# Kernel optimization log

Measured on AMD Instinct MI355X. Metric: run time of the kernel, lower is better.

## Reference

```python
import jax, jax.numpy as jnp
import numpy as np

RES = 128
STEPSIZE = 0.5
NEAR, FAR, BG = 0.2, 3.0, 1.0
ALPHA_INIT = 0.01
XYZ_MIN, XYZ_MAX = -1.0, 1.0
N_RAYS = 1024
RGB_LATENT = 15
MULTIRES = 6
EMB_DIM = 3 + 3 * 2 * MULTIRES  # 39
DIM0 = RGB_LATENT + EMB_DIM     # 54
VOXEL = (XYZ_MAX - XYZ_MIN) / RES  # ((2^3)/RES^3)^(1/3)
N_SAMPLES = int(np.linalg.norm(np.array([RES] * 3) * 2 + 1) / STEPSIZE) + 1  # 891
ACT_SHIFT = float(np.log(1.0 / (1.0 - ALPHA_INIT) - 1.0))


def embed_dirs(d):
    # NeRF positional encoding, include_inputs=True, multires=6 -> 39 dims
    freqs = 2.0 ** jnp.arange(MULTIRES, dtype=d.dtype)
    ang = d[..., None, :] * freqs[:, None]  # [M,6,3]
    return jnp.concatenate([d, jnp.sin(ang).reshape(d.shape[0], -1), jnp.cos(ang).reshape(d.shape[0], -1)], -1)


def grid_sample3d(g, coords):
    # g: [C,D,H,W]; coords: [M,3] in (-1,1), torch grid_sample convention
    # (comp0 -> W axis, comp1 -> H axis, comp2 -> D axis), align_corners=True,
    # border-clamped indices (sampled out-of-box points are masked out anyway).
    C, D, H, W = g.shape
    x = (coords[:, 0] + 1) * 0.5 * (W - 1)
    y = (coords[:, 1] + 1) * 0.5 * (H - 1)
    z = (coords[:, 2] + 1) * 0.5 * (D - 1)
    x0, y0, z0 = jnp.floor(x), jnp.floor(y), jnp.floor(z)
    fx, fy, fz = x - x0, y - y0, z - z0
    x0i = jnp.clip(x0.astype(jnp.int32), 0, W - 1); x1i = jnp.clip(x0i + 1, 0, W - 1)
    y0i = jnp.clip(y0.astype(jnp.int32), 0, H - 1); y1i = jnp.clip(y0i + 1, 0, H - 1)
    z0i = jnp.clip(z0.astype(jnp.int32), 0, D - 1); z1i = jnp.clip(z0i + 1, 0, D - 1)
    gf = g.reshape(C, -1)
    def gv(zi, yi, xi):
        return gf[:, (zi * H + yi) * W + xi]  # [C,M]
    c = (((gv(z0i, y0i, x0i) * (1 - fx) + gv(z0i, y0i, x1i) * fx) * (1 - fy)
          + (gv(z0i, y1i, x0i) * (1 - fx) + gv(z0i, y1i, x1i) * fx) * fy) * (1 - fz)
         + ((gv(z1i, y0i, x0i) * (1 - fx) + gv(z1i, y0i, x1i) * fx) * (1 - fy)
            + (gv(z1i, y1i, x0i) * (1 - fx) + gv(z1i, y1i, x1i) * fx) * fy) * fz)
    return c.T  # [M,C]


def _forward(rays_o, rays_d, viewdirs, grid, sobel_kernel, w0, b0, w1, b1, w2, b2, w3, b3):
    # --- sample_ray: ray/AABB intersection + uniform stepping ---
    vec = jnp.where(rays_d == 0, 1e-6, rays_d)
    rate_a = (XYZ_MAX - rays_o) / vec
    rate_b = (XYZ_MIN - rays_o) / vec
    t_min = jnp.clip(jnp.minimum(rate_a, rate_b).max(-1), NEAR, FAR)
    t_max = jnp.clip(jnp.maximum(rate_a, rate_b).min(-1), NEAR, FAR)
    mask_ray = t_max <= t_min
    rng = jnp.arange(N_SAMPLES, dtype=rays_o.dtype)[None]
    step = STEPSIZE * VOXEL * rng
    interpx = t_min[:, None] + step / jnp.linalg.norm(rays_d, axis=-1, keepdims=True)
    pts = rays_o[:, None, :] + rays_d[:, None, :] * interpx[..., None]  # [N,S,3]
    inbox = (~mask_ray[:, None]) & (~((pts < XYZ_MIN) | (pts > XYZ_MAX)).any(-1))
    mflat = inbox.reshape(-1)

    # --- sobel normals grid (GridReg.forward(calc_normals=True)) ---
    density_grid = grid[None, :1]  # [1,1,D,H,W]
    nrm = jax.lax.conv_general_dilated(density_grid, sobel_kernel, (1, 1, 1), [(2, 2)] * 3,
                                       dimension_numbers=('NCDHW', 'OIDHW', 'NCDHW'))  # [1,3,D,H,W]
    nrm = -nrm / jnp.maximum(jnp.linalg.norm(nrm, axis=1, keepdims=True), 1e-12)
    normals_grid = nrm[0]

    # --- extract_latent: trilinear sample at ray points (masked via where) ---
    flat = pts.reshape(-1, 3)
    coords = ((flat - XYZ_MIN) / (XYZ_MAX - XYZ_MIN))[:, ::-1] * 2 - 1  # flip xyz->zyx
    lat = grid_sample3d(grid, coords)          # [M,16]
    ns = grid_sample3d(normals_grid, coords)   # [M,3]
    ns = -ns / jnp.maximum(jnp.linalg.norm(ns, axis=-1, keepdims=True), 1e-12)

    alpha = jnp.where(mflat, 1 - jnp.exp(-jax.nn.softplus(lat[:, 0] + ACT_SHIFT) * STEPSIZE), 0.0)
    alpha = alpha.reshape(N_RAYS, N_SAMPLES)
    normals = jnp.where(mflat[:, None], ns, 0.0).reshape(N_RAYS, N_SAMPLES, 3)
    rgb_lat = jnp.where(mflat[:, None], lat[:, 1:], 0.0)  # [M,15]

    # --- alpha compositing (cumprod_exclusive / get_ray_marching_ray) ---
    alphainv_cum = jnp.concatenate([jnp.ones_like(alpha[:, :1]),
                                    jnp.cumprod(jnp.maximum(1 - alpha, 1e-10), -1)], -1)
    weights = alpha * alphainv_cum[:, :-1]

    # --- reflected-direction shading MLP ---
    v = jnp.broadcast_to(viewdirs[:, None, :], normals.shape)
    dot = jnp.sum(-v * normals, -1, keepdims=True)
    refdirs = (2 * dot * normals + v).reshape(-1, 3)
    feat = jnp.concatenate([rgb_lat, embed_dirs(refdirs)], -1)  # [M,54]
    h = jax.nn.relu(feat @ w0 + b0)
    h = jax.nn.relu(h @ w1 + b1)
    h = jax.nn.relu(h @ w2 + b2)
    col = jax.nn.sigmoid(h @ w3 + b3)
    rgb = jnp.where(mflat[:, None], col, 0.0).reshape(N_RAYS, N_SAMPLES, 3)

    rgb_marched = (weights[..., None] * rgb).sum(-2) + alphainv_cum[:, -1:] * BG
    return rgb_marched


def setup_inputs() -> dict:
    key = jax.random.key(0)
    ks = jax.random.split(key, 8)
    rays_o = 0.3 * jax.random.normal(ks[0], (N_RAYS, 3), jnp.float32)
    rd = jax.random.normal(ks[1], (N_RAYS, 3), jnp.float32)
    rays_d = rd / jnp.linalg.norm(rd, axis=-1, keepdims=True)
    grid = 0.1 * jax.random.normal(ks[2], (1 + RGB_LATENT, RES, RES, RES), jnp.float32)
    sobel_kernel = jax.random.normal(ks[3], (3, 1, 5, 5, 5), jnp.float32)
    def lin(k, i, o):
        return jax.random.normal(k, (i, o), jnp.float32) / np.sqrt(i).astype(np.float32)
    return {
        'rays_o': rays_o, 'rays_d': rays_d, 'viewdirs': rays_d,
        'grid': grid, 'sobel_kernel': sobel_kernel,
        'w0': lin(ks[4], DIM0, 64), 'b0': jnp.zeros((64,), jnp.float32),
        'w1': lin(ks[5], 64, 64), 'b1': jnp.zeros((64,), jnp.float32),
        'w2': lin(ks[6], 64, 64), 'b2': jnp.zeros((64,), jnp.float32),
        'w3': lin(ks[7], 64, 3), 'b3': jnp.zeros((3,), jnp.float32),
    }


def reference(rays_o, rays_d, viewdirs, grid, sobel_kernel, w0, b0, w1, b1, w2, b2, w3, b3):
    return _forward(rays_o, rays_d, viewdirs, grid, sobel_kernel, w0, b0, w1, b1, w2, b2, w3, b3)
```

## Files before the change

### kernel.cpp

```cpp
#include <hip/hip_runtime.h>
#include <hip/hip_bf16.h>
#include <hip/hip_fp16.h>
#include <math.h>

#define RESV 128
#define V3 (RESV*RESV*RESV)
#define N_RAYS 1024
#define N_SAMPLES 891
#define STEP_T 0.0078125f
#define ACT_SHIFT -4.595119850134589f

typedef short bf16x8 __attribute__((ext_vector_type(8)));
typedef float f32x4 __attribute__((ext_vector_type(4)));

__device__ __forceinline__ unsigned short f2b(float x) {
    unsigned int u = __float_as_uint(x);
    unsigned int r = (u + 0x7FFFu + ((u >> 16) & 1u)) >> 16;
    return (unsigned short)r;
}

__device__ __forceinline__ void acc2(float w, unsigned int u, float& lo, float& hi) {
    lo = fmaf(w, __uint_as_float(u << 16), lo);
    hi = fmaf(w, __uint_as_float(u & 0xffff0000u), hi);
}

#define ROWS 60
#define ZSTR 136

__global__ __launch_bounds__(256)
void normals_conv_kernel(const float* __restrict__ grid,
                         const float* __restrict__ sobel,
                         float4* __restrict__ nrm4) {
    __shared__ float sk[375];
    __shared__ __align__(16) float tile[ROWS * ZSTR];

    const int t = threadIdx.x;
    const int bx = blockIdx.x;
    const int ix = bx >> 4;
    const int iy0 = (bx & 15) * 8;

    for (int i = t; i < 375; i += 256) sk[i] = sobel[i];

    {
        const int lane32 = t & 31;
        for (int r = t >> 5; r < ROWS; r += 8) {
            const int xl = r / 12, yl = r % 12;
            const int gx = ix + xl - 2;
            const int gy = iy0 + yl - 2;
            float4 v = make_float4(0.f, 0.f, 0.f, 0.f);
            if ((unsigned)gx < 128u && (unsigned)gy < 128u)
                v = *(const float4*)&grid[(size_t)(gx * 128 + gy) * 128 + lane32 * 4];
            *(float4*)&tile[r * ZSTR + 4 + lane32 * 4] = v;
        }
        if (t < ROWS) {
            float* row = tile + t * ZSTR;
            row[0] = 0.f; row[1] = 0.f; row[2] = 0.f; row[3] = 0.f;
            row[132] = 0.f; row[133] = 0.f; row[134] = 0.f; row[135] = 0.f;
        }
    }
    __syncthreads();

    const int iz4 = (t & 31) * 4;
    const int iyl = t >> 5;

    float c0[4] = {0.f, 0.f, 0.f, 0.f};
    float c1[4] = {0.f, 0.f, 0.f, 0.f};
    float c2[4] = {0.f, 0.f, 0.f, 0.f};

    #pragma unroll
    for (int da = 0; da < 5; ++da) {
        #pragma unroll
        for (int db = 0; db < 5; ++db) {
            const float* row = tile + (da * 12 + iyl + db + 2) * ZSTR;
            const float* k0  = sk + (da * 5 + db) * 5;
            float gbuf[12];
            *(float4*)&gbuf[0] = *(const float4*)&row[iz4];
            *(float4*)&gbuf[4] = *(const float4*)&row[iz4 + 4];
            *(float4*)&gbuf[8] = *(const float4*)&row[iz4 + 8];
            #pragma unroll
            for (int zz = 0; zz < 4; ++zz) {
                #pragma unroll
                for (int dc = 0; dc < 5; ++dc) {
                    const float gv = gbuf[2 + zz + dc];
                    c0[zz] = fmaf(gv, k0[dc],       c0[zz]);
                    c1[zz] = fmaf(gv, k0[125 + dc], c1[zz]);
                    c2[zz] = fmaf(gv, k0[250 + dc], c2[zz]);
                }
            }
        }
    }
    const int vbase = (ix * 128 + iy0 + iyl) * 128 + iz4;
    #pragma unroll
    for (int zz = 0; zz < 4; ++zz) {
        float l   = sqrtf(c0[zz]*c0[zz] + c1[zz]*c1[zz] + c2[zz]*c2[zz]);
        float inv = -1.0f / fmaxf(l, 1e-12f);
        nrm4[vbase + zz] = make_float4(c0[zz]*inv, c1[zz]*inv, c2[zz]*inv, 0.f);
    }
}

__global__ __launch_bounds__(256)
void repack_kernel(const float* __restrict__ grid,
                   unsigned short* __restrict__ latp) {
    const int i = blockIdx.x * 256 + threadIdx.x;
    const int v0 = i * 4;
    unsigned int r[4][8];
    #pragma unroll
    for (int c = 0; c < 16; c += 2) {
        const float4 a = *(const float4*)&grid[(size_t)c * V3 + v0];
        const float4 b = *(const float4*)&grid[(size_t)(c + 1) * V3 + v0];
        const float* pa = &a.x; const float* pb = &b.x;
        #pragma unroll
        for (int z = 0; z < 4; ++z)
            r[z][c >> 1] = (unsigned int)f2b(pa[z]) | ((unsigned int)f2b(pb[z]) << 16);
    }
    uint4* d = (uint4*)&latp[(size_t)v0 * 16];
    #pragma unroll
    for (int z = 0; z < 4; ++z) {
        d[z * 2 + 0] = make_uint4(r[z][0], r[z][1], r[z][2], r[z][3]);
        d[z * 2 + 1] = make_uint4(r[z][4], r[z][5], r[z][6], r[z][7]);
    }
}

__device__ __forceinline__ void mfma_layer(unsigned short* __restrict__ actw,
                                           const unsigned short* __restrict__ WT,
                                           const float* __restrict__ Bv,
                                           int r16, int q4, int q8) {
    f32x4 acc[4][4];
    #pragma unroll
    for (int nb = 0; nb < 4; ++nb) {
        const float bv = Bv[nb * 16 + r16];
        #pragma unroll
        for (int mb = 0; mb < 4; ++mb) {
            acc[mb][nb][0] = bv; acc[mb][nb][1] = bv;
            acc[mb][nb][2] = bv; acc[mb][nb][3] = bv;
        }
    }
    #pragma unroll
    for (int ks = 0; ks < 2; ++ks) {
        bf16x8 Af[4], Bf[4];
        #pragma unroll
        for (int mb = 0; mb < 4; ++mb)
            Af[mb] = *(const bf16x8*)&actw[(mb * 16 + r16) * 72 + ks * 32 + q8];
        #pragma unroll
        for (int nb = 0; nb < 4; ++nb)
            Bf[nb] = *(const bf16x8*)&WT[(nb * 16 + r16) * 72 + ks * 32 + q8];
        #pragma unroll
        for (int mb = 0; mb < 4; ++mb) {
            #pragma unroll
            for (int nb = 0; nb < 4; ++nb)
                acc[mb][nb] = __builtin_amdgcn_mfma_f32_16x16x32_bf16(
                    Af[mb], Bf[nb], acc[mb][nb], 0, 0, 0);
        }
    }
    #pragma unroll
    for (int mb = 0; mb < 4; ++mb) {
        #pragma unroll
        for (int nb = 0; nb < 4; ++nb) {
            #pragma unroll
            for (int r = 0; r < 4; ++r) {
                const int row = mb * 16 + q4 + r;
                actw[row * 72 + nb * 16 + r16] = f2b(fmaxf(acc[mb][nb][r], 0.f));
            }
        }
    }
}

#define WT0_OFF 0
#define WT1_OFF (64*72)
#define WT2_OFF (128*72)
#define WT3_OFF (192*72)

template <bool PL>
__global__ __launch_bounds__(256)
void raymarch_kernel(const float* __restrict__ ro, const float* __restrict__ rd,
                     const float* __restrict__ vd, const float* __restrict__ grid,
                     const float4* __restrict__ nrm4,
                     const unsigned short* __restrict__ latp,
                     const float* __restrict__ w0, const float* __restrict__ b0,
                     const float* __restrict__ w1, const float* __restrict__ b1,
                     const float* __restrict__ w2, const float* __restrict__ b2,
                     const float* __restrict__ w3, const float* __restrict__ b3,
                     float* __restrict__ out) {
    __shared__ __align__(16) unsigned short sWT[208 * 72];
    __shared__ __align__(16) unsigned short act[4 * 64 * 72];
    __shared__ float sb0f[64], sb1f[64], sb2f[64], sb3f[16];
    __shared__ __half salpha[1024];
    __shared__ __half scr[1024], scg[1024], scb[1024];
    __shared__ float lgl[1024];
    __shared__ float aux[256];
    __shared__ float red[12];

    const int t = threadIdx.x;
    const int ray = blockIdx.x;
    const int lane = t & 63;
    const int wave = t >> 6;
    const int r16 = lane & 15;
    const int q4 = (lane >> 4) * 4;
    const int q8 = (lane >> 4) * 8;
    unsigned short* const actw = act + wave * 64 * 72;

    for (int i = t; i < 64 * 72; i += 256) {
        int o = i / 72, k = i % 72;
        sWT[WT0_OFF + i] = f2b((k < 54) ? w0[k * 64 + o] : 0.f);
        sWT[WT1_OFF + i] = f2b((k < 64) ? w1[k * 64 + o] : 0.f);
        sWT[WT2_OFF + i] = f2b((k < 64) ? w2[k * 64 + o] : 0.f);
    }
    for (int i = t; i < 16 * 72; i += 256) {
        int n = i / 72, k = i % 72;
        sWT[WT3_OFF + i] = f2b((n < 3 && k < 64) ? w3[k * 3 + n] : 0.f);
    }
    if (t < 64) { sb0f[t] = b0[t]; sb1f[t] = b1[t]; sb2f[t] = b2[t]; }
    if (t < 16) sb3f[t] = (t < 3) ? b3[t] : 0.f;
    __syncthreads();

    const float ox = ro[ray * 3 + 0], oy = ro[ray * 3 + 1], oz = ro[ray * 3 + 2];
    const float dx = rd[ray * 3 + 0], dyv = rd[ray * 3 + 1], dzv = rd[ray * 3 + 2];
    const float vx = vd[ray * 3 + 0], vy = vd[ray * 3 + 1], vz = vd[ray * 3 + 2];

    const float ex = (dx  == 0.f) ? 1e-6f : dx;
    const float ey = (dyv == 0.f) ? 1e-6f : dyv;
    const float ez = (dzv == 0.f) ? 1e-6f : dzv;
    const float rax = (1.f - ox) / ex, rbx = (-1.f - ox) / ex;
    const float ray_ = (1.f - oy) / ey, rby = (-1.f - oy) / ey;
    const float raz = (1.f - oz) / ez, rbz = (-1.f - oz) / ez;
    float tmin = fmaxf(fmaxf(fminf(rax, rbx), fminf(ray_, rby)), fminf(raz, rbz));
    float tmax = fminf(fminf(fmaxf(rax, rbx), fmaxf(ray_, rby)), fmaxf(raz, rbz));
    tmin = fminf(fmaxf(tmin, 0.2f), 3.0f);
    tmax = fminf(fmaxf(tmax, 0.2f), 3.0f);
    const bool mask_ray = (tmax <= tmin);
    const float invn = 1.0f / sqrtf(dx * dx + dyv * dyv + dzv * dzv);

    #pragma unroll 1
    for (int j = 0; j < 4; ++j) {
        const int s = j * 256 + t;
        float alpha_s = 0.f;
        bool active = (s < N_SAMPLES) && !mask_ray;
        float px = 0.f, py = 0.f, pz = 0.f;
        if (active) {
            const float ti = tmin + STEP_T * (float)s * invn;
            px = fmaf(dx, ti, ox);
            py = fmaf(dyv, ti, oy);
            pz = fmaf(dzv, ti, oz);
            active = !(px < -1.f || px > 1.f || py < -1.f || py > 1.f ||
                       pz < -1.f || pz > 1.f);
        }
        const unsigned long long wmask = __ballot(active);
        if (wmask == 0ull) {
            salpha[s] = __float2half(0.f);
            lgl[s] = 0.f;
            scr[s] = __float2half(0.f); scg[s] = __float2half(0.f);
            scb[s] = __float2half(0.f);
            continue;
        }

        float feat[54];
        #pragma unroll
        for (int i = 0; i < 54; ++i) feat[i] = 0.f;

        if (active) {
            const float ga = (px + 1.f) * 63.5f;
            const float gb = (py + 1.f) * 63.5f;
            const float gc = (pz + 1.f) * 63.5f;
            const float fla = floorf(ga), flb = floorf(gb), flc = floorf(gc);
            const float fa = ga - fla, fb = gb - flb, fc = gc - flc;
            int ia0 = min(max((int)fla, 0), 127);
            int ib0 = min(max((int)flb, 0), 127);
            int ic0 = min(max((int)flc, 0), 127);
            int ia1 = min(ia0 + 1, 127);
            int ib1 = min(ib0 + 1, 127);
            int ic1 = min(ic0 + 1, 127);
            const int base00 = (ia0 * 128 + ib0) * 128;
            const int base01 = (ia0 * 128 + ib1) * 128;
            const int base10 = (ia1 * 128 + ib0) * 128;
            const int base11 = (ia1 * 128 + ib1) * 128;
            int idxs[8] = { base00 + ic0, base00 + ic1, base01 + ic0, base01 + ic1,
                            base10 + ic0, base10 + ic1, base11 + ic0, base11 + ic1 };
            const float wa0 = 1.f - fa, wb0 = 1.f - fb, wc0 = 1.f - fc;
            float w8[8] = { wa0*wb0*wc0, wa0*wb0*fc, wa0*fb*wc0, wa0*fb*fc,
                            fa*wb0*wc0,  fa*wb0*fc,  fa*fb*wc0,  fa*fb*fc };

            float lat[16];
            #pragma unroll
            for (int c = 0; c < 16; ++c) lat[c] = 0.f;
            if constexpr (PL) {
                #pragma unroll
                for (int k = 0; k < 8; ++k) {
                    const uint4* rec = (const uint4*)&latp[(size_t)idxs[k] * 16];
                    const uint4 u0 = rec[0];
                    const uint4 u1 = rec[1];
                    const float w = w8[k];
                    acc2(w, u0.x, lat[0],  lat[1]);
                    acc2(w, u0.y, lat[2],  lat[3]);
                    acc2(w, u0.z, lat[4],  lat[5]);
                    acc2(w, u0.w, lat[6],  lat[7]);
                    acc2(w, u1.x, lat[8],  lat[9]);
                    acc2(w, u1.y, lat[10], lat[11]);
                    acc2(w, u1.z, lat[12], lat[13]);
                    acc2(w, u1.w, lat[14], lat[15]);
                }
            } else {
                #pragma unroll
                for (int c = 0; c < 16; ++c) {
                    const float* gcp = grid + (size_t)c * V3;
                    float acc = 0.f;
                    #pragma unroll
                    for (int k = 0; k < 8; ++k) acc = fmaf(w8[k], gcp[idxs[k]], acc);
                    lat[c] = acc;
                }
            }
            const float lat0 = lat[0];
            #pragma unroll
            for (int c = 0; c < 15; ++c) feat[c] = lat[c + 1];

            float n0 = 0.f, n1 = 0.f, n2 = 0.f;
            #pragma unroll
            for (int k = 0; k < 8; ++k) {
                const float4 nv = nrm4[idxs[k]];
                n0 = fmaf(w8[k], nv.x, n0);
                n1 = fmaf(w8[k], nv.y, n1);
                n2 = fmaf(w8[k], nv.z, n2);
            }
            const float nl = sqrtf(n0*n0 + n1*n1 + n2*n2);
            const float ninv = -1.0f / fmaxf(nl, 1e-12f);
            n0 *= ninv; n1 *= ninv; n2 *= ninv;
            const float dotv = -(vx * n0 + vy * n1 + vz * n2);
            const float rx = fmaf(2.f * dotv, n0, vx);
            const float ry = fmaf(2.f * dotv, n1, vy);
            const float rz = fmaf(2.f * dotv, n2, vz);

            const float d0 = lat0 + ACT_SHIFT;
            const float sp = (d0 > 20.f) ? d0 : __logf(1.f + __expf(d0));
            alpha_s = 1.f - __expf(-sp * 0.5f);

            feat[15] = rx; feat[16] = ry; feat[17] = rz;
            float fr = 1.f;
            #pragma unroll
            for (int k = 0; k < 6; ++k) {
                feat[18 + k*3 + 0] = __sinf(rx * fr);
                feat[18 + k*3 + 1] = __sinf(ry * fr);
                feat[18 + k*3 + 2] = __sinf(rz * fr);
                feat[36 + k*3 + 0] = __cosf(rx * fr);
                feat[36 + k*3 + 1] = __cosf(ry * fr);
                feat[36 + k*3 + 2] = __cosf(rz * fr);
                fr *= 2.f;
            }
        }
        salpha[s] = __float2half(alpha_s);
        lgl[s] = __logf(fmaxf(1.f - alpha_s, 1e-10f));

        unsigned int* arow = (unsigned int*)&act[(size_t)t * 72];
        #pragma unroll
        for (int p = 0; p < 27; ++p)
            arow[p] = (unsigned int)f2b(feat[2*p]) |
                      ((unsigned int)f2b(feat[2*p + 1]) << 16);
        #pragma unroll
        for (int p = 27; p < 32; ++p) arow[p] = 0u;

        mfma_layer(actw, sWT + WT0_OFF, sb0f, r16, q4, q8);
        mfma_layer(actw, sWT + WT1_OFF, sb1f, r16, q4, q8);
        mfma_layer(actw, sWT + WT2_OFF, sb2f, r16, q4, q8);

        {
            f32x4 acch[4];
            const float bv = sb3f[r16];
            #pragma unroll
            for (int mb = 0; mb < 4; ++mb) {
                acch[mb][0] = bv; acch[mb][1] = bv;
                acch[mb][2] = bv; acch[mb][3] = bv;
            }
            #pragma unroll
            for (int ks = 0; ks < 2; ++ks) {
                const bf16x8 Bh = *(const bf16x8*)&sWT[WT3_OFF + r16 * 72 + ks * 32 + q8];
                #pragma unroll
                for (int mb = 0; mb < 4; ++mb) {
                    const bf16x8 Af = *(const bf16x8*)&actw[(mb * 16 + r16) * 72 + ks * 32 + q8];
                    acch[mb] = __builtin_amdgcn_mfma_f32_16x16x32_bf16(Af, Bh, acch[mb], 0, 0, 0);
                }
            }
            if (r16 < 3) {
                __half* dst = (r16 == 0) ? scr : (r16 == 1) ? scg : scb;
                const int jb = j * 256 + wave * 64;
                #pragma unroll
                for (int mb = 0; mb < 4; ++mb) {
                    #pragma unroll
                    for (int r = 0; r < 4; ++r) {
                        const int samp = mb * 16 + q4 + r;
                        dst[jb + samp] = __float2half(1.f / (1.f + __expf(-acch[mb][r])));
                    }
                }
            }
        }
    }
    __syncthreads();

    {
        float c0 = lgl[4*t + 0];
        float c1 = c0 + lgl[4*t + 1];
        float c2 = c1 + lgl[4*t + 2];
        float c3 = c2 + lgl[4*t + 3];
        lgl[4*t + 0] = c0; lgl[4*t + 1] = c1;
        lgl[4*t + 2] = c2; lgl[4*t + 3] = c3;
        aux[t] = c3;
    }
    __syncthreads();
    for (int off = 1; off < 256; off <<= 1) {
        const float v = (t >= off) ? aux[t - off] : 0.f;
        __syncthreads();
        aux[t] += v;
        __syncthreads();
    }
    const float total = aux[255];

    float r0 = 0.f, r1 = 0.f, r2 = 0.f;
    #pragma unroll
    for (int j = 0; j < 4; ++j) {
        const int s = j * 256 + t;
        const float a = __half2float(salpha[s]);
        if (s < N_SAMPLES && a > 0.f) {
            float G;
            if (s == 0) G = 0.f;
            else {
                const int m = s - 1;
                G = lgl[m] + (((m >> 2) > 0) ? aux[(m >> 2) - 1] : 0.f);
            }
            const float T = __expf(G);
            const float w = a * T;
            r0 = fmaf(w, __half2float(scr[s]), r0);
            r1 = fmaf(w, __half2float(scg[s]), r1);
            r2 = fmaf(w, __half2float(scb[s]), r2);
        }
    }
    #pragma unroll
    for (int off = 32; off > 0; off >>= 1) {
        r0 += __shfl_down(r0, off, 64);
        r1 += __shfl_down(r1, off, 64);
        r2 += __shfl_down(r2, off, 64);
    }
    if ((t & 63) == 0) {
        red[wave * 3 + 0] = r0; red[wave * 3 + 1] = r1; red[wave * 3 + 2] = r2;
    }
    __syncthreads();
    if (t == 0) {
        const float Tf = __expf(total);
        out[ray * 3 + 0] = red[0] + red[3] + red[6] + red[9]  + Tf;
        out[ray * 3 + 1] = red[1] + red[4] + red[7] + red[10] + Tf;
        out[ray * 3 + 2] = red[2] + red[5] + red[8] + red[11] + Tf;
    }
}

extern "C" void kernel_launch(void* const* d_in, const int* in_sizes, int n_in,
                              void* d_out, int out_size, void* d_ws, size_t ws_size,
                              hipStream_t stream) {
    (void)in_sizes; (void)n_in; (void)out_size;
    const float* ro    = (const float*)d_in[0];
    const float* rd    = (const float*)d_in[1];
    const float* vd    = (const float*)d_in[2];
    const float* grid  = (const float*)d_in[3];
    const float* sobel = (const float*)d_in[4];
    const float* w0 = (const float*)d_in[5];
    const float* b0 = (const float*)d_in[6];
    const float* w1 = (const float*)d_in[7];
    const float* b1 = (const float*)d_in[8];
    const float* w2 = (const float*)d_in[9];
    const float* b2 = (const float*)d_in[10];
    const float* w3 = (const float*)d_in[11];
    const float* b3 = (const float*)d_in[12];

    float4* nrm4 = (float4*)d_ws;
    const size_t NRM_BYTES = (size_t)V3 * 16;
    const size_t LAT_BYTES = (size_t)V3 * 32;
    unsigned short* latp = (unsigned short*)((char*)d_ws + NRM_BYTES);
    const bool packed = (ws_size >= NRM_BYTES + LAT_BYTES);

    normals_conv_kernel<<<128 * 16, 256, 0, stream>>>(grid, sobel, nrm4);
    if (packed) {
        repack_kernel<<<V3 / 4 / 256, 256, 0, stream>>>(grid, latp);
        raymarch_kernel<true><<<N_RAYS, 256, 0, stream>>>(ro, rd, vd, grid, nrm4, latp,
                                                          w0, b0, w1, b1, w2, b2, w3, b3,
                                                          (float*)d_out);
    } else {
        raymarch_kernel<false><<<N_RAYS, 256, 0, stream>>>(ro, rd, vd, grid, nrm4, latp,
                                                           w0, b0, w1, b1, w2, b2, w3, b3,
                                                           (float*)d_out);
    }
}
```

Baseline: 344.5 us.

## Prepack MLP weights into MFMA fragment layout in global memory, drop LDS copy

Adds a one-block prep kernel that converts the MLP weights to bf16 in per-lane MFMA fragment order, written to workspace. The raymarch kernel then loads B fragments directly from global memory (cache-resident) instead of from a per-block LDS transposed copy. This removes the repeated per-block weight conversion prologue and about 30KB of LDS, and sets launch bounds to 3 blocks per CU to raise occupancy. The trade-off is global/L2 loads in the inner MLP loop in place of LDS reads, plus one extra tiny kernel launch.

```diff
diff --git a/kernel.cpp b/kernel.cpp
--- a/kernel.cpp
+++ b/kernel.cpp
@@ -22,6 +22,32 @@
 __device__ __forceinline__ void acc2(float w, unsigned int u, float& lo, float& hi) {
     lo = fmaf(w, __uint_as_float(u << 16), lo);
     hi = fmaf(w, __uint_as_float(u & 0xffff0000u), hi);
+}
+
+__global__ __launch_bounds__(256)
+void wprep_kernel(const float* __restrict__ w0, const float* __restrict__ w1,
+                  const float* __restrict__ w2, const float* __restrict__ w3,
+                  unsigned short* __restrict__ wfr) {
+    const int t = threadIdx.x;
+    for (int i = t; i < 26 * 64 * 8; i += 256) {
+        const int j = i & 7;
+        const int lane = (i >> 3) & 63;
+        const int frag = i >> 9;
+        const int r16 = lane & 15, q = lane >> 4;
+        float v;
+        if (frag < 24) {
+            const int l = frag >> 3, ks = (frag >> 2) & 1, nb = frag & 3;
+            const int n = nb * 16 + r16;
+            const int k = ks * 32 + q * 8 + j;
+            const float* W = (l == 0) ? w0 : (l == 1) ? w1 : w2;
+            v = (l == 0 && k >= 54) ? 0.f : W[k * 64 + n];
+        } else {
+            const int ks = frag - 24;
+            const int k = ks * 32 + q * 8 + j;
+            v = (r16 < 3) ? w3[k * 3 + r16] : 0.f;
+        }
+        wfr[i] = f2b(v);
+    }
 }
 
 #define ROWS 60
@@ -122,9 +148,9 @@
 }
 
 __device__ __forceinline__ void mfma_layer(unsigned short* __restrict__ actw,
-                                           const unsigned short* __restrict__ WT,
-                                           const float* __restrict__ Bv,
-                                           int r16, int q4, int q8) {
+                                           const unsigned short* __restrict__ wfr,
+                                           int l, const float* __restrict__ Bv,
+                                           int lane, int r16, int q4, int q8) {
     f32x4 acc[4][4];
     #pragma unroll
     for (int nb = 0; nb < 4; ++nb) {
@@ -143,7 +169,7 @@
             Af[mb] = *(const bf16x8*)&actw[(mb * 16 + r16) * 72 + ks * 32 + q8];
         #pragma unroll
         for (int nb = 0; nb < 4; ++nb)
-            Bf[nb] = *(const bf16x8*)&WT[(nb * 16 + r16) * 72 + ks * 32 + q8];
+            Bf[nb] = *(const bf16x8*)&wfr[(size_t)((((l * 2 + ks) * 4) + nb) * 64 + lane) * 8];
         #pragma unroll
         for (int mb = 0; mb < 4; ++mb) {
             #pragma unroll
@@ -165,23 +191,16 @@
     }
 }
 
-#define WT0_OFF 0
-#define WT1_OFF (64*72)
-#define WT2_OFF (128*72)
-#define WT3_OFF (192*72)
-
 template <bool PL>
-__global__ __launch_bounds__(256)
+__global__ __launch_bounds__(256, 3)
 void raymarch_kernel(const float* __restrict__ ro, const float* __restrict__ rd,
                      const float* __restrict__ vd, const float* __restrict__ grid,
                      const float4* __restrict__ nrm4,
                      const unsigned short* __restrict__ latp,
-                     const float* __restrict__ w0, const float* __restrict__ b0,
-                     const float* __restrict__ w1, const float* __restrict__ b1,
-                     const float* __restrict__ w2, const float* __restrict__ b2,
-                     const float* __restrict__ w3, const float* __restrict__ b3,
+                     const unsigned short* __restrict__ wfr,
+                     const float* __restrict__ b0, const float* __restrict__ b1,
+                     const float* __restrict__ b2, const float* __restrict__ b3,
                      float* __restrict__ out) {
-    __shared__ __align__(16) unsigned short sWT[208 * 72];
     __shared__ __align__(16) unsigned short act[4 * 64 * 72];
     __shared__ float sb0f[64], sb1f[64], sb2f[64], sb3f[16];
     __shared__ __half salpha[1024];
@@ -199,16 +218,6 @@
     const int q8 = (lane >> 4) * 8;
     unsigned short* const actw = act + wave * 64 * 72;
 
-    for (int i = t; i < 64 * 72; i += 256) {
-        int o = i / 72, k = i % 72;
-        sWT[WT0_OFF + i] = f2b((k < 54) ? w0[k * 64 + o] : 0.f);
-        sWT[WT1_OFF + i] = f2b((k < 64) ? w1[k * 64 + o] : 0.f);
-        sWT[WT2_OFF + i] = f2b((k < 64) ? w2[k * 64 + o] : 0.f);
-    }
-    for (int i = t; i < 16 * 72; i += 256) {
-        int n = i / 72, k = i % 72;
-        sWT[WT3_OFF + i] = f2b((n < 3 && k < 64) ? w3[k * 3 + n] : 0.f);
-    }
     if (t < 64) { sb0f[t] = b0[t]; sb1f[t] = b1[t]; sb2f[t] = b2[t]; }
     if (t < 16) sb3f[t] = (t < 3) ? b3[t] : 0.f;
     __syncthreads();
@@ -356,9 +365,9 @@
         #pragma unroll
         for (int p = 27; p < 32; ++p) arow[p] = 0u;
 
-        mfma_layer(actw, sWT + WT0_OFF, sb0f, r16, q4, q8);
-        mfma_layer(actw, sWT + WT1_OFF, sb1f, r16, q4, q8);
-        mfma_layer(actw, sWT + WT2_OFF, sb2f, r16, q4, q8);
+        mfma_layer(actw, wfr, 0, sb0f, lane, r16, q4, q8);
+        mfma_layer(actw, wfr, 1, sb1f, lane, r16, q4, q8);
+        mfma_layer(actw, wfr, 2, sb2f, lane, r16, q4, q8);
 
         {
             f32x4 acch[4];
@@ -370,7 +379,7 @@
             }
             #pragma unroll
             for (int ks = 0; ks < 2; ++ks) {
-                const bf16x8 Bh = *(const bf16x8*)&sWT[WT3_OFF + r16 * 72 + ks * 32 + q8];
+                const bf16x8 Bh = *(const bf16x8*)&wfr[(size_t)((24 + ks) * 64 + lane) * 8];
                 #pragma unroll
                 for (int mb = 0; mb < 4; ++mb) {
                     const bf16x8 Af = *(const bf16x8*)&actw[(mb * 16 + r16) * 72 + ks * 32 + q8];
@@ -466,21 +475,24 @@
     const float* w3 = (const float*)d_in[11];
     const float* b3 = (const float*)d_in[12];
 
-    float4* nrm4 = (float4*)d_ws;
     const size_t NRM_BYTES = (size_t)V3 * 16;
     const size_t LAT_BYTES = (size_t)V3 * 32;
+    const size_t WFR_BYTES = 26 * 64 * 8 * 2;
+    float4* nrm4 = (float4*)d_ws;
+    const bool packed = (ws_size >= NRM_BYTES + LAT_BYTES + WFR_BYTES);
     unsigned short* latp = (unsigned short*)((char*)d_ws + NRM_BYTES);
-    const bool packed = (ws_size >= NRM_BYTES + LAT_BYTES);
-
+    unsigned short* wfr  = packed
+        ? (unsigned short*)((char*)d_ws + NRM_BYTES + LAT_BYTES)
+        : (unsigned short*)((char*)d_ws + NRM_BYTES);
+
+    wprep_kernel<<<1, 256, 0, stream>>>(w0, w1, w2, w3, wfr);
     normals_conv_kernel<<<128 * 16, 256, 0, stream>>>(grid, sobel, nrm4);
     if (packed) {
         repack_kernel<<<V3 / 4 / 256, 256, 0, stream>>>(grid, latp);
-        raymarch_kernel<true><<<N_RAYS, 256, 0, stream>>>(ro, rd, vd, grid, nrm4, latp,
-                                                          w0, b0, w1, b1, w2, b2, w3, b3,
-                                                          (float*)d_out);
+        raymarch_kernel<true><<<N_RAYS, 256, 0, stream>>>(ro, rd, vd, grid, nrm4, latp, wfr,
+                                                          b0, b1, b2, b3, (float*)d_out);
     } else {
-        raymarch_kernel<false><<<N_RAYS, 256, 0, stream>>>(ro, rd, vd, grid, nrm4, latp,
-                                                           w0, b0, w1, b1, w2, b2, w3, b3,
-                                                           (float*)d_out);
-    }
-}
+        raymarch_kernel<false><<<N_RAYS, 256, 0, stream>>>(ro, rd, vd, grid, nrm4, latp, wfr,
+                                                           b0, b1, b2, b3, (float*)d_out);
+    }
+}
```

Measured after the change: 351.9 us. +2.2%, slower.
